# Optimization experiments

Hardware: AMD Instinct MI355X
Metric: run time of the kernel (lower is better)

## Reference

```python
import jax, jax.numpy as jnp
import numpy as np

B, L, W, H = 4, 4096, 2560, 10  # batch, seq_len, width, num_heads
BW = W // H                      # block width of BlockDiagonalLinear


def _block_linear(x, w, b):
    # x: [B, L, W] -> [B, L, H, BW]; block-diagonal matmul per head.
    xr = x.reshape(x.shape[0], x.shape[1], H, BW)
    y = jnp.einsum('blhi,hij->blhj', xr, w) + b
    return y.reshape(x.shape)


def setup_inputs() -> dict:
    key = jax.random.key(0)
    k_x, k_wx, k_wa, k_a = jax.random.split(key, 4)
    x = jax.random.normal(k_x, (B, L, W), dtype=jnp.float32)
    # One document per sequence: positions 0..L-1 (reset only at t=0).
    segment_pos = jnp.tile(jnp.arange(L, dtype=jnp.int32)[None, :], (B, 1))
    # BlockDiagonalLinear params: variance_scaling(fan_in, normal).
    std = 1.0 / np.sqrt(BW)
    w_x = jax.random.normal(k_wx, (H, BW, BW), dtype=jnp.float32) * std
    b_x = jnp.zeros((H, BW), dtype=jnp.float32)
    w_a = jax.random.normal(k_wa, (H, BW, BW), dtype=jnp.float32) * std
    b_a = jnp.zeros((H, BW), dtype=jnp.float32)
    # a_param: ring init on [0.9, 0.999], softplus-transformed.
    min_rad, max_rad, eps = 0.9, 0.999, 1e-8
    unif = jax.random.uniform(k_a, (W,))
    a_real = 0.5 * jnp.log(unif * (max_rad**2 - min_rad**2) + min_rad**2 + eps)
    a_param = jnp.log(jnp.exp(-a_real) - 1.0).astype(jnp.float32)
    return {'x': x, 'segment_pos': segment_pos, 'a_param': a_param,
            'w_x': w_x, 'b_x': b_x, 'w_a': w_a, 'b_a': b_a}


def reference(x, segment_pos, a_param, w_x, b_x, w_a, b_a):
    reset = (segment_pos == 0)                       # [B, L] bool
    r = reset[..., None].astype(x.dtype)             # [B, L, 1]

    gate_x = jax.nn.sigmoid(_block_linear(x, w_x, b_x))
    gate_a = jax.nn.sigmoid(_block_linear(x, w_a, b_a))

    log_a = -8.0 * gate_a * jax.nn.softplus(a_param)  # [B, L, W]
    a = jnp.exp(log_a)
    a_squared = jnp.exp(2.0 * log_a)

    multiplier = jnp.sqrt(1.0 - a_squared)            # sqrt_bound_derivative fwd == sqrt
    multiplier = r + (1.0 - r) * multiplier
    normalized_x = x * gate_x * multiplier

    a = a * (1.0 - r)                                 # reset masking of decay

    # Diagonal linear recurrence h_t = a_t * h_{t-1} + x_t via associative scan.
    def binop(ei, ej):
        a_i, bu_i = ei
        a_j, bu_j = ej
        return a_j * a_i, a_j * bu_i + bu_j

    _, y = jax.lax.associative_scan(
        binop, (a.astype(jnp.float32), normalized_x.astype(jnp.float32)), axis=1)
    return y.astype(x.dtype), y[:, -1]
```

## Files before the change

### kernel.cpp

```cpp
#include <hip/hip_runtime.h>
#include <hip/hip_bf16.h>
#include <math.h>

#define B_ 4
#define L_ 4096
#define W_ 2560
#define H_ 10
#define NC_ 64
#define TRANGE 256
#define AL_STRIDE 266

typedef __attribute__((ext_vector_type(8))) short bf16x8;
typedef __attribute__((ext_vector_type(4))) float f32x4;
typedef __attribute__((ext_vector_type(4))) unsigned short u16x4;

#define L2E 1.44269504088896f

__device__ inline unsigned short f2bf(float f){
  unsigned u = __builtin_bit_cast(unsigned, f);
  u += 0x7fffu + ((u >> 16) & 1u);
  return (unsigned short)(u >> 16);
}
__device__ inline float bf2f(unsigned short s){
  unsigned u = (unsigned)s << 16;
  return __builtin_bit_cast(float, u);
}
__device__ inline float fast_rcp(float x){
#if __has_builtin(__builtin_amdgcn_rcpf)
  return __builtin_amdgcn_rcpf(x);
#else
  return 1.f / x;
#endif
}
__device__ inline float fast_sqrt(float x){
#if __has_builtin(__builtin_amdgcn_sqrtf)
  return __builtin_amdgcn_sqrtf(x);
#else
  return sqrtf(x);
#endif
}
__device__ inline float fast_sigmoid(float z){
  return fast_rcp(1.f + exp2f(-z * L2E));
}

__global__ __launch_bounds__(256) void k_prep(
    const float* __restrict__ w_x, const float* __restrict__ w_a,
    const float* __restrict__ a_param,
    unsigned short* __restrict__ Wt, float* __restrict__ sp_buf){
  int idx = blockIdx.x * 256 + threadIdx.x;
  if (idx < H_ * 512 * 256){
    int k = idx & 255;
    int n = (idx >> 8) & 511;
    int h = idx >> 17;
    float v = (n < 256) ? w_x[((size_t)h * 256 + k) * 256 + n]
                        : w_a[((size_t)h * 256 + k) * 256 + (n - 256)];
    Wt[idx] = f2bf(v);
  }
  if (idx < W_) sp_buf[idx] = -8.f * L2E * log1pf(expf(a_param[idx]));
}

__global__ __launch_bounds__(512, 4) void k_gates(
    const float* __restrict__ x, const int* __restrict__ segpos,
    const unsigned short* __restrict__ Wt,
    const float* __restrict__ b_x, const float* __restrict__ b_a,
    const float* __restrict__ sp_buf,
    unsigned* __restrict__ pk_buf,
    float* __restrict__ P_buf, float* __restrict__ S_buf){
  __shared__ alignas(16) unsigned short Al[16 * AL_STRIDE];

  const int bid   = blockIdx.x;
  const int range = bid & 15;
  const int half  = (bid >> 4) & 1;
  const int rest  = bid >> 5;
  const int h     = rest % H_;
  const int b     = rest / H_;
  const int t_base = range * TRANGE;

  const int tid  = threadIdx.x;
  const int wave = tid >> 6, lane = tid & 63;
  const int lr = lane & 15, hi = lane >> 4;
  const int c_loc = half * 128 + wave * 16 + lr;
  const int cg    = h * 256 + c_loc;

  const unsigned short* Wh = Wt + (size_t)h * 512 * 256;
  bf16x8 bfx[8], bfa[8];
  #pragma unroll
  for (int k8 = 0; k8 < 8; k8++){
    bfx[k8] = *(const bf16x8*)(Wh + (size_t)c_loc * 256 + k8 * 32 + hi * 8);
    bfa[k8] = *(const bf16x8*)(Wh + (size_t)(c_loc + 256) * 256 + k8 * 32 + hi * 8);
  }
  const float bxv = b_x[h * 256 + c_loc];
  const float bav = b_a[h * 256 + c_loc];
  const float sp2 = sp_buf[cg];

  const float* xh = x + ((size_t)b * L_ + t_base) * W_ + h * 256;
  const f32x4 zero = {0.f, 0.f, 0.f, 0.f};

  float Pch = 1.f, Sch = 0.f;

  for (int tile = 0; tile < TRANGE / 16; tile++){
    __syncthreads();
    #pragma unroll
    for (int rep = 0; rep < 2; rep++){
      int Q = tid + rep * 512;
      int row = Q >> 6, kq = Q & 63;
      float4 v = *(const float4*)(xh + (size_t)(tile * 16 + row) * W_ + kq * 4);
      u16x4 p; p.x = f2bf(v.x); p.y = f2bf(v.y); p.z = f2bf(v.z); p.w = f2bf(v.w);
      *(u16x4*)&Al[row * AL_STRIDE + kq * 4] = p;
    }
    __syncthreads();

    f32x4 accx = zero, acca = zero;
    #pragma unroll
    for (int k8 = 0; k8 < 8; k8++){
      bf16x8 af = *(const bf16x8*)&Al[lr * AL_STRIDE + k8 * 32 + hi * 8];
      accx = __builtin_amdgcn_mfma_f32_16x16x32_bf16(af, bfx[k8], accx, 0, 0, 0);
      acca = __builtin_amdgcn_mfma_f32_16x16x32_bf16(af, bfa[k8], acca, 0, 0, 0);
    }

    float Pseg = 1.f, Sseg = 0.f;
    #pragma unroll
    for (int i = 0; i < 4; i++){
      const int t = t_base + tile * 16 + hi * 4 + i;
      const size_t o = ((size_t)b * L_ + t) * W_ + cg;
      const int seg = segpos[b * L_ + t];
      float gx = fast_sigmoid(accx[i] + bxv);
      float ga = fast_sigmoid(acca[i] + bav);
      float la2 = sp2 * ga;
      float av = exp2f(la2);
      float mult = fast_sqrt(fmaf(-av, av, 1.f));
      if (seg == 0){ av = 0.f; mult = 1.f; la2 = -INFINITY; }
      float xb = bf2f(Al[(hi * 4 + i) * AL_STRIDE + c_loc]);
      float nxv = xb * gx * mult;
      unsigned pk = ((unsigned)f2bf(nxv) << 16) | (unsigned)f2bf(la2);
      pk_buf[o] = pk;
      Sseg = fmaf(av, Sseg, nxv);
      Pseg *= av;
    }
    {
      float Po = __shfl_xor(Pseg, 16);
      float So = __shfl_xor(Sseg, 16);
      Sseg = (hi & 1) ? fmaf(Pseg, So, Sseg) : fmaf(Po, Sseg, So);
      Pseg = Pseg * Po;
      Po = __shfl_xor(Pseg, 32);
      So = __shfl_xor(Sseg, 32);
      Sseg = ((hi >> 1) & 1) ? fmaf(Pseg, So, Sseg) : fmaf(Po, Sseg, So);
      Pseg = Pseg * Po;
    }
    Sch = fmaf(Pseg, Sch, Sseg);
    Pch = Pch * Pseg;
    if ((tile & 3) == 3){
      if (hi == 0){
        const int chunk = (t_base >> 6) + (tile >> 2);
        const size_t po = ((size_t)b * NC_ + chunk) * W_ + cg;
        P_buf[po] = Pch;
        S_buf[po] = Sch;
      }
      Pch = 1.f; Sch = 0.f;
    }
  }
}

__global__ __launch_bounds__(256) void k_scanB(
    const float* __restrict__ P_buf, const float* __restrict__ S_buf,
    float* __restrict__ carry_buf, float* __restrict__ y_last){
  const int g = blockIdx.x * 256 + threadIdx.x;
  const int b = g / (W_ / 2), c2 = g % (W_ / 2);
  float2 carry = {0.f, 0.f};
  size_t off = (size_t)b * NC_ * (W_ / 2) + c2;
  const float2* P2 = (const float2*)P_buf;
  const float2* S2 = (const float2*)S_buf;
  float2* C2 = (float2*)carry_buf;
  for (int ch = 0; ch < NC_; ch++){
    C2[off] = carry;
    float2 P = P2[off], S = S2[off];
    carry.x = fmaf(P.x, carry.x, S.x);
    carry.y = fmaf(P.y, carry.y, S.y);
    off += W_ / 2;
  }
  *(float2*)&y_last[(size_t)b * W_ + c2 * 2] = carry;
}

__global__ __launch_bounds__(320) void k_scanC(
    const unsigned* __restrict__ pk_buf, const float* __restrict__ carry_buf,
    float* __restrict__ y){
  const int bid  = blockIdx.x;
  const int half = bid & 1;
  const int ch   = (bid >> 1) % NC_;
  const int b    = bid / (2 * NC_);
  const int c4 = half * (W_ / 2) + threadIdx.x * 4;
  float4 hc = *(const float4*)&carry_buf[((size_t)b * NC_ + ch) * W_ + c4];
  size_t off = ((size_t)b * L_ + ch * 64) * W_ + c4;
  #pragma unroll 4
  for (int t = 0; t < 64; t++){
    uint4 pk = *(const uint4*)&pk_buf[off];
    float4 out;
    {
      float a  = exp2f(__builtin_bit_cast(float, pk.x << 16));
      float nx = __builtin_bit_cast(float, pk.x & 0xFFFF0000u);
      out.x = hc.x = fmaf(a, hc.x, nx);
    }
    {
      float a  = exp2f(__builtin_bit_cast(float, pk.y << 16));
      float nx = __builtin_bit_cast(float, pk.y & 0xFFFF0000u);
      out.y = hc.y = fmaf(a, hc.y, nx);
    }
    {
      float a  = exp2f(__builtin_bit_cast(float, pk.z << 16));
      float nx = __builtin_bit_cast(float, pk.z & 0xFFFF0000u);
      out.z = hc.z = fmaf(a, hc.z, nx);
    }
    {
      float a  = exp2f(__builtin_bit_cast(float, pk.w << 16));
      float nx = __builtin_bit_cast(float, pk.w & 0xFFFF0000u);
      out.w = hc.w = fmaf(a, hc.w, nx);
    }
    *(float4*)&y[off] = out;
    off += W_;
  }
}

extern "C" void kernel_launch(void* const* d_in, const int* in_sizes, int n_in,
                              void* d_out, int out_size, void* d_ws, size_t ws_size,
                              hipStream_t stream){
  (void)in_sizes; (void)n_in; (void)out_size; (void)ws_size;
  const float* x       = (const float*)d_in[0];
  const int*   segpos  = (const int*)d_in[1];
  const float* a_param = (const float*)d_in[2];
  const float* w_x     = (const float*)d_in[3];
  const float* b_x     = (const float*)d_in[4];
  const float* w_a     = (const float*)d_in[5];
  const float* b_a     = (const float*)d_in[6];

  float* y      = (float*)d_out;
  float* y_last = y + (size_t)B_ * L_ * W_;

  char* p = (char*)d_ws;
  unsigned* pk_buf = (unsigned*)p;          p += (size_t)B_ * L_ * W_ * 4;
  unsigned short* Wt = (unsigned short*)p;  p += (size_t)H_ * 512 * 256 * 2;
  float* sp_buf = (float*)p;                p += (size_t)W_ * 4;
  float* P_buf = (float*)p;                 p += (size_t)B_ * NC_ * W_ * 4;
  float* S_buf = (float*)p;                 p += (size_t)B_ * NC_ * W_ * 4;
  float* carry_buf = (float*)p;             p += (size_t)B_ * NC_ * W_ * 4;

  k_prep<<<dim3((H_ * 512 * 256 + 255) / 256), dim3(256), 0, stream>>>(
      w_x, w_a, a_param, Wt, sp_buf);
  k_gates<<<dim3(B_ * H_ * 2 * (L_ / TRANGE)), dim3(512), 0, stream>>>(
      x, segpos, Wt, b_x, b_a, sp_buf, pk_buf, P_buf, S_buf);
  k_scanB<<<dim3((B_ * W_ / 2) / 256), dim3(256), 0, stream>>>(
      P_buf, S_buf, carry_buf, y_last);
  k_scanC<<<dim3(B_ * NC_ * 2), dim3(320), 0, stream>>>(
      pk_buf, carry_buf, y);
}
```

Before: 442.5 us.

## Compute intra-range scan in gates kernel and apply carry in elementwise pass

The gates kernel now computes the full local scan within each 256-step range, storing the local prefix y and the cumulative log-decay packed as bf16 pairs. The final pass becomes a parallel elementwise correction y = exp2(L)*carry + y_local, done in place in the output buffer. This removes the serial 64-step rescan and the separate workspace buffer. It also widens tiles to 32 rows per MFMA step and cuts the chunk count to 16. The trade-off is that the local y is stored in bf16 and cumulative logs are summed over long ranges, which risks precision loss. Occupancy also drops to 3 blocks.

```diff
diff --git a/kernel.cpp b/kernel.cpp
--- a/kernel.cpp
+++ b/kernel.cpp
@@ -6,24 +6,23 @@
 #define L_ 4096
 #define W_ 2560
 #define H_ 10
-#define NC_ 64
+#define NC_ 16
 #define TRANGE 256
-#define AL_STRIDE 266
+#define AL_STRIDE 268
 
 typedef __attribute__((ext_vector_type(8))) short bf16x8;
 typedef __attribute__((ext_vector_type(4))) float f32x4;
-typedef __attribute__((ext_vector_type(4))) unsigned short u16x4;
 
 #define L2E 1.44269504088896f
 
+__device__ inline float bf2f(unsigned short s){
+  unsigned u = (unsigned)s << 16;
+  return __builtin_bit_cast(float, u);
+}
 __device__ inline unsigned short f2bf(float f){
   unsigned u = __builtin_bit_cast(unsigned, f);
   u += 0x7fffu + ((u >> 16) & 1u);
   return (unsigned short)(u >> 16);
-}
-__device__ inline float bf2f(unsigned short s){
-  unsigned u = (unsigned)s << 16;
-  return __builtin_bit_cast(float, u);
 }
 __device__ inline float fast_rcp(float x){
 #if __has_builtin(__builtin_amdgcn_rcpf)
@@ -41,6 +40,9 @@
 }
 __device__ inline float fast_sigmoid(float z){
   return fast_rcp(1.f + exp2f(-z * L2E));
+}
+__device__ inline unsigned pack_bf2(float lo, float hi){
+  return ((unsigned)f2bf(hi) << 16) | (unsigned)f2bf(lo);
 }
 
 __global__ __launch_bounds__(256) void k_prep(
@@ -59,14 +61,14 @@
   if (idx < W_) sp_buf[idx] = -8.f * L2E * log1pf(expf(a_param[idx]));
 }
 
-__global__ __launch_bounds__(512, 4) void k_gates(
+__global__ __launch_bounds__(512, 3) void k_gates(
     const float* __restrict__ x, const int* __restrict__ segpos,
     const unsigned short* __restrict__ Wt,
     const float* __restrict__ b_x, const float* __restrict__ b_a,
     const float* __restrict__ sp_buf,
     unsigned* __restrict__ pk_buf,
     float* __restrict__ P_buf, float* __restrict__ S_buf){
-  __shared__ alignas(16) unsigned short Al[16 * AL_STRIDE];
+  __shared__ alignas(16) unsigned short Al[32 * AL_STRIDE];
 
   const int bid   = blockIdx.x;
   const int range = bid & 15;
@@ -92,72 +94,91 @@
   const float bxv = b_x[h * 256 + c_loc];
   const float bav = b_a[h * 256 + c_loc];
   const float sp2 = sp_buf[cg];
+  asm volatile("" ::: "memory");
 
   const float* xh = x + ((size_t)b * L_ + t_base) * W_ + h * 256;
   const f32x4 zero = {0.f, 0.f, 0.f, 0.f};
 
-  float Pch = 1.f, Sch = 0.f;
-
-  for (int tile = 0; tile < TRANGE / 16; tile++){
+  float Pch = 1.f, Sch = 0.f, Lch = 0.f;
+
+  for (int ss = 0; ss < TRANGE / 32; ss++){
     __syncthreads();
     #pragma unroll
-    for (int rep = 0; rep < 2; rep++){
+    for (int rep = 0; rep < 4; rep++){
       int Q = tid + rep * 512;
       int row = Q >> 6, kq = Q & 63;
-      float4 v = *(const float4*)(xh + (size_t)(tile * 16 + row) * W_ + kq * 4);
-      u16x4 p; p.x = f2bf(v.x); p.y = f2bf(v.y); p.z = f2bf(v.z); p.w = f2bf(v.w);
-      *(u16x4*)&Al[row * AL_STRIDE + kq * 4] = p;
+      float4 v = *(const float4*)(xh + (size_t)(ss * 32 + row) * W_ + kq * 4);
+      uint2 st = { pack_bf2(v.x, v.y), pack_bf2(v.z, v.w) };
+      *(uint2*)&Al[row * AL_STRIDE + kq * 4] = st;
     }
     __syncthreads();
 
-    f32x4 accx = zero, acca = zero;
+    f32x4 accx[2] = {zero, zero}, acca[2] = {zero, zero};
     #pragma unroll
     for (int k8 = 0; k8 < 8; k8++){
-      bf16x8 af = *(const bf16x8*)&Al[lr * AL_STRIDE + k8 * 32 + hi * 8];
-      accx = __builtin_amdgcn_mfma_f32_16x16x32_bf16(af, bfx[k8], accx, 0, 0, 0);
-      acca = __builtin_amdgcn_mfma_f32_16x16x32_bf16(af, bfa[k8], acca, 0, 0, 0);
+      #pragma unroll
+      for (int m = 0; m < 2; m++){
+        union { bf16x8 v; uint2 u[2]; } af;
+        const int off = (m * 16 + lr) * AL_STRIDE + k8 * 32 + hi * 8;
+        af.u[0] = *(const uint2*)&Al[off];
+        af.u[1] = *(const uint2*)&Al[off + 4];
+        accx[m] = __builtin_amdgcn_mfma_f32_16x16x32_bf16(af.v, bfx[k8], accx[m], 0, 0, 0);
+        acca[m] = __builtin_amdgcn_mfma_f32_16x16x32_bf16(af.v, bfa[k8], acca[m], 0, 0, 0);
+      }
     }
 
-    float Pseg = 1.f, Sseg = 0.f;
     #pragma unroll
-    for (int i = 0; i < 4; i++){
-      const int t = t_base + tile * 16 + hi * 4 + i;
-      const size_t o = ((size_t)b * L_ + t) * W_ + cg;
-      const int seg = segpos[b * L_ + t];
-      float gx = fast_sigmoid(accx[i] + bxv);
-      float ga = fast_sigmoid(acca[i] + bav);
-      float la2 = sp2 * ga;
-      float av = exp2f(la2);
-      float mult = fast_sqrt(fmaf(-av, av, 1.f));
-      if (seg == 0){ av = 0.f; mult = 1.f; la2 = -INFINITY; }
-      float xb = bf2f(Al[(hi * 4 + i) * AL_STRIDE + c_loc]);
-      float nxv = xb * gx * mult;
-      unsigned pk = ((unsigned)f2bf(nxv) << 16) | (unsigned)f2bf(la2);
-      pk_buf[o] = pk;
-      Sseg = fmaf(av, Sseg, nxv);
-      Pseg *= av;
+    for (int m = 0; m < 2; m++){
+      float av[4], nxv[4], la2v[4];
+      float gp = 1.f, gs = 0.f, gl = 0.f;
+      #pragma unroll
+      for (int i = 0; i < 4; i++){
+        const int trow = m * 16 + hi * 4 + i;
+        const int t = t_base + ss * 32 + trow;
+        const int seg = segpos[b * L_ + t];
+        float gx = fast_sigmoid(accx[m][i] + bxv);
+        float ga = fast_sigmoid(acca[m][i] + bav);
+        float l2 = sp2 * ga;
+        float a  = exp2f(l2);
+        float mult = fast_sqrt(fmaf(-a, a, 1.f));
+        if (seg == 0){ a = 0.f; mult = 1.f; l2 = -INFINITY; }
+        float xb = bf2f(Al[trow * AL_STRIDE + c_loc]);
+        float nx = xb * gx * mult;
+        av[i] = a; nxv[i] = nx; la2v[i] = l2;
+        gs = fmaf(a, gs, nx); gp *= a; gl += l2;
+      }
+      float a1p = __shfl_xor(gp, 16), a1s = __shfl_xor(gs, 16), a1l = __shfl_xor(gl, 16);
+      float pp = gp * a1p;
+      float ps = (hi & 1) ? fmaf(a1s, gp, gs) : fmaf(gs, a1p, a1s);
+      float pl = gl + a1l;
+      float bp = __shfl_xor(pp, 32), bs = __shfl_xor(ps, 32), bl = __shfl_xor(pl, 32);
+      float exP = (hi == 0) ? 1.f : (hi == 1) ? a1p : (hi == 2) ? bp : bp * a1p;
+      float exS = (hi == 0) ? 0.f : (hi == 1) ? a1s : (hi == 2) ? bs : fmaf(bs, a1p, a1s);
+      float exL = (hi == 0) ? 0.f : (hi == 1) ? a1l : (hi == 2) ? bl : bl + a1l;
+      float cS = fmaf(Sch, exP, exS);
+      float cL = Lch + exL;
+      float pc = 1.f, sc = 0.f, lc = 0.f;
+      #pragma unroll
+      for (int i = 0; i < 4; i++){
+        pc *= av[i]; sc = fmaf(av[i], sc, nxv[i]); lc += la2v[i];
+        float yv = fmaf(pc, cS, sc);
+        float lg = lc + cL;
+        const int t = t_base + ss * 32 + m * 16 + hi * 4 + i;
+        pk_buf[((size_t)b * L_ + t) * W_ + cg] = pack_bf2(lg, yv);
+      }
+      float totP = pp * bp;
+      float totS = (hi < 2) ? fmaf(ps, bp, bs) : fmaf(bs, pp, ps);
+      float totL = pl + bl;
+      Sch = fmaf(Sch, totP, totS);
+      Pch = Pch * totP;
+      Lch = Lch + totL;
     }
-    {
-      float Po = __shfl_xor(Pseg, 16);
-      float So = __shfl_xor(Sseg, 16);
-      Sseg = (hi & 1) ? fmaf(Pseg, So, Sseg) : fmaf(Po, Sseg, So);
-      Pseg = Pseg * Po;
-      Po = __shfl_xor(Pseg, 32);
-      So = __shfl_xor(Sseg, 32);
-      Sseg = ((hi >> 1) & 1) ? fmaf(Pseg, So, Sseg) : fmaf(Po, Sseg, So);
-      Pseg = Pseg * Po;
-    }
-    Sch = fmaf(Pseg, Sch, Sseg);
-    Pch = Pch * Pseg;
-    if ((tile & 3) == 3){
-      if (hi == 0){
-        const int chunk = (t_base >> 6) + (tile >> 2);
-        const size_t po = ((size_t)b * NC_ + chunk) * W_ + cg;
-        P_buf[po] = Pch;
-        S_buf[po] = Sch;
-      }
-      Pch = 1.f; Sch = 0.f;
-    }
+  }
+
+  if (hi == 0){
+    const size_t po = ((size_t)b * NC_ + range) * W_ + cg;
+    P_buf[po] = Pch;
+    S_buf[po] = Sch;
   }
 }
 
@@ -165,58 +186,40 @@
     const float* __restrict__ P_buf, const float* __restrict__ S_buf,
     float* __restrict__ carry_buf, float* __restrict__ y_last){
   const int g = blockIdx.x * 256 + threadIdx.x;
-  const int b = g / (W_ / 2), c2 = g % (W_ / 2);
-  float2 carry = {0.f, 0.f};
-  size_t off = (size_t)b * NC_ * (W_ / 2) + c2;
-  const float2* P2 = (const float2*)P_buf;
-  const float2* S2 = (const float2*)S_buf;
-  float2* C2 = (float2*)carry_buf;
+  const int b = g / W_, c = g % W_;
+  float carry = 0.f;
+  size_t off = (size_t)b * NC_ * W_ + c;
+  #pragma unroll
   for (int ch = 0; ch < NC_; ch++){
-    C2[off] = carry;
-    float2 P = P2[off], S = S2[off];
-    carry.x = fmaf(P.x, carry.x, S.x);
-    carry.y = fmaf(P.y, carry.y, S.y);
-    off += W_ / 2;
-  }
-  *(float2*)&y_last[(size_t)b * W_ + c2 * 2] = carry;
-}
-
-__global__ __launch_bounds__(320) void k_scanC(
-    const unsigned* __restrict__ pk_buf, const float* __restrict__ carry_buf,
-    float* __restrict__ y){
-  const int bid  = blockIdx.x;
-  const int half = bid & 1;
-  const int ch   = (bid >> 1) % NC_;
-  const int b    = bid / (2 * NC_);
-  const int c4 = half * (W_ / 2) + threadIdx.x * 4;
-  float4 hc = *(const float4*)&carry_buf[((size_t)b * NC_ + ch) * W_ + c4];
-  size_t off = ((size_t)b * L_ + ch * 64) * W_ + c4;
-  #pragma unroll 4
-  for (int t = 0; t < 64; t++){
-    uint4 pk = *(const uint4*)&pk_buf[off];
-    float4 out;
-    {
-      float a  = exp2f(__builtin_bit_cast(float, pk.x << 16));
-      float nx = __builtin_bit_cast(float, pk.x & 0xFFFF0000u);
-      out.x = hc.x = fmaf(a, hc.x, nx);
-    }
-    {
-      float a  = exp2f(__builtin_bit_cast(float, pk.y << 16));
-      float nx = __builtin_bit_cast(float, pk.y & 0xFFFF0000u);
-      out.y = hc.y = fmaf(a, hc.y, nx);
-    }
-    {
-      float a  = exp2f(__builtin_bit_cast(float, pk.z << 16));
-      float nx = __builtin_bit_cast(float, pk.z & 0xFFFF0000u);
-      out.z = hc.z = fmaf(a, hc.z, nx);
-    }
-    {
-      float a  = exp2f(__builtin_bit_cast(float, pk.w << 16));
-      float nx = __builtin_bit_cast(float, pk.w & 0xFFFF0000u);
-      out.w = hc.w = fmaf(a, hc.w, nx);
-    }
-    *(float4*)&y[off] = out;
+    carry_buf[off] = carry;
+    carry = fmaf(P_buf[off], carry, S_buf[off]);
     off += W_;
+  }
+  y_last[g] = carry;
+}
+
+__global__ __launch_bounds__(256) void k_scanC(
+    unsigned* pky,
+    const float* __restrict__ carry_buf){
+  const unsigned total4 = B_ * L_ * (W_ / 4);
+  const unsigned stride = gridDim.x * blockDim.x;
+  for (unsigned g = blockIdx.x * blockDim.x + threadIdx.x; g < total4; g += stride){
+    unsigned c4 = g % (W_ / 4);
+    unsigned bt = g / (W_ / 4);
+    unsigned t = bt & (L_ - 1);
+    unsigned b = bt >> 12;
+    uint4 pk = ((const uint4*)pky)[g];
+    float4 cr = *(const float4*)&carry_buf[((size_t)b * NC_ + (t >> 8)) * W_ + c4 * 4];
+    float4 yv;
+    yv.x = fmaf(exp2f(__builtin_bit_cast(float, pk.x << 16)), cr.x,
+                __builtin_bit_cast(float, pk.x & 0xFFFF0000u));
+    yv.y = fmaf(exp2f(__builtin_bit_cast(float, pk.y << 16)), cr.y,
+                __builtin_bit_cast(float, pk.y & 0xFFFF0000u));
+    yv.z = fmaf(exp2f(__builtin_bit_cast(float, pk.z << 16)), cr.z,
+                __builtin_bit_cast(float, pk.z & 0xFFFF0000u));
+    yv.w = fmaf(exp2f(__builtin_bit_cast(float, pk.w << 16)), cr.w,
+                __builtin_bit_cast(float, pk.w & 0xFFFF0000u));
+    ((float4*)pky)[g] = yv;
   }
 }
 
@@ -234,9 +237,9 @@
 
   float* y      = (float*)d_out;
   float* y_last = y + (size_t)B_ * L_ * W_;
+  unsigned* pk_buf = (unsigned*)d_out;
 
   char* p = (char*)d_ws;
-  unsigned* pk_buf = (unsigned*)p;          p += (size_t)B_ * L_ * W_ * 4;
   unsigned short* Wt = (unsigned short*)p;  p += (size_t)H_ * 512 * 256 * 2;
   float* sp_buf = (float*)p;                p += (size_t)W_ * 4;
   float* P_buf = (float*)p;                 p += (size_t)B_ * NC_ * W_ * 4;
@@ -245,10 +248,10 @@
 
   k_prep<<<dim3((H_ * 512 * 256 + 255) / 256), dim3(256), 0, stream>>>(
       w_x, w_a, a_param, Wt, sp_buf);
-  k_gates<<<dim3(B_ * H_ * 2 * (L_ / TRANGE)), dim3(512), 0, stream>>>(
+  k_gates<<<dim3(B_ * H_ * 2 * NC_), dim3(512), 0, stream>>>(
       x, segpos, Wt, b_x, b_a, sp_buf, pk_buf, P_buf, S_buf);
-  k_scanB<<<dim3((B_ * W_ / 2) / 256), dim3(256), 0, stream>>>(
+  k_scanB<<<dim3((B_ * W_) / 256), dim3(256), 0, stream>>>(
       P_buf, S_buf, carry_buf, y_last);
-  k_scanC<<<dim3(B_ * NC_ * 2), dim3(320), 0, stream>>>(
-      pk_buf, carry_buf, y);
-}
+  k_scanC<<<dim3(2048), dim3(256), 0, stream>>>(
+      pk_buf, carry_buf);
+}
```

After: 475.3 us. +7.4%, slower.
